# Kernel optimization log

Hardware: AMD Instinct MI355X
Metric: run time of the kernel (lower is better)

## Reference

```python
import jax, jax.numpy as jnp
import numpy as np

# architecture (from init_kwargs): layer_widths = [1024, 512, 512, 512]
D0, D1, D2, D3 = 1024, 512, 512, 512
D = D1 + D2 + D3  # flat DEQ state dim = 1536
M_AA = 5          # anderson history size
LAM = 1e-4        # tikhonov reg in least-squares
THRES = 50        # hard-coded in DeepDEQAutoencoder.forward
BETA = 1.0


def enc(z, Y, W1, W2, W3):
    """Encoder f(z, Y): z_l_new = relu(W_l @ z_{l-1}), z_0 = Y. z is [B, D]."""
    z1 = z[:, :D1]
    z2 = z[:, D1:D1 + D2]
    n1 = jax.nn.relu(Y @ W1.T)   # [B, D1]
    n2 = jax.nn.relu(z1 @ W2.T)  # [B, D2]
    n3 = jax.nn.relu(z2 @ W3.T)  # [B, D3]
    return jnp.concatenate([n1, n2, n3], axis=1)


def anderson(f, x0, m=M_AA, lam=LAM, threshold=THRES, beta=BETA):
    """Standard DEQ Anderson acceleration, fixed `threshold` iterations."""
    B, d = x0.shape
    X = jnp.zeros((B, m, d), x0.dtype)
    F = jnp.zeros((B, m, d), x0.dtype)
    f0 = f(x0)
    X = X.at[:, 0].set(x0)
    F = F.at[:, 0].set(f0)
    X = X.at[:, 1].set(f0)
    F = F.at[:, 1].set(f(f0))
    for k in range(2, threshold):
        n = min(k, m)
        G = F[:, :n] - X[:, :n]                                  # [B, n, d]
        H = jnp.einsum('bnd,bmd->bnm', G, G) + lam * jnp.eye(n, dtype=x0.dtype)
        # bordered system: [[0, 1^T], [1, H]] alpha_full = e_0
        top = jnp.concatenate([jnp.zeros((B, 1, 1), x0.dtype),
                               jnp.ones((B, 1, n), x0.dtype)], axis=2)
        bot = jnp.concatenate([jnp.ones((B, n, 1), x0.dtype), H], axis=2)
        Hf = jnp.concatenate([top, bot], axis=1)                 # [B, n+1, n+1]
        yv = jnp.zeros((B, n + 1, 1), x0.dtype).at[:, 0, 0].set(1.0)
        alpha = jnp.linalg.solve(Hf, yv)[:, 1:, 0]               # [B, n]
        xk = beta * jnp.einsum('bn,bnd->bd', alpha, F[:, :n]) \
             + (1.0 - beta) * jnp.einsum('bn,bnd->bd', alpha, X[:, :n])
        X = X.at[:, k % m].set(xk)
        F = F.at[:, k % m].set(f(xk))
    return F[:, (threshold - 1) % m]


def setup_inputs() -> dict:
    key = jax.random.key(0)
    ks = jax.random.split(key, 7)
    # weight scale 0.03 keeps the relu network contractive so the fixed point is stable
    return {
        'Y':  jax.random.normal(ks[0], (4096, D0), jnp.float32),
        'W1': jax.random.normal(ks[1], (D1, D0), jnp.float32) * 0.03,
        'W2': jax.random.normal(ks[2], (D2, D1), jnp.float32) * 0.03,
        'W3': jax.random.normal(ks[3], (D3, D2), jnp.float32) * 0.03,
        'b1': jax.random.normal(ks[4], (D0,), jnp.float32) * 0.01,
        'b2': jax.random.normal(ks[5], (D1,), jnp.float32) * 0.01,
        'b3': jax.random.normal(ks[6], (D2,), jnp.float32) * 0.01,
    }


def reference(Y, W1, W2, W3, b1, b2, b3):
    B = Y.shape[0]
    z0 = jnp.zeros((B, D), Y.dtype)
    z_star = anderson(lambda z: enc(z, Y, W1, W2, W3), z0)
    # eval mode: new_f_star = f_star; return calc_all_etas(f_star)
    z1 = z_star[:, :D1]
    z2 = z_star[:, D1:D1 + D2]
    z3 = z_star[:, D1 + D2:]
    eta1 = z1 @ W1 + b1  # linear(z_l, M_l.weight.T, biases[l]) == z_l @ W_l + b_l
    eta2 = z2 @ W2 + b2
    eta3 = z3 @ W3 + b3
    # (etas, zs) packed into one array along features: [B, 1024+512+512 + 1536]
    return jnp.concatenate([eta1, eta2, eta3, z1, z2, z3], axis=1)
```

## Files before the change

### kernel.cpp

```cpp
#include <hip/hip_runtime.h>
#include <hip/hip_bf16.h>
#include <cstdint>

#define OUT_LD 3584

typedef __bf16 bf16x8 __attribute__((ext_vector_type(8)));
typedef float  f32x4  __attribute__((ext_vector_type(4)));

__device__ __forceinline__ short f2bf(float v) {
  __hip_bfloat16 h = __float2bfloat16(v);
  return *reinterpret_cast<short*>(&h);
}

__device__ __forceinline__ void async16(const short* g, short* l) {
  __builtin_amdgcn_global_load_lds(
      (const __attribute__((address_space(1))) unsigned int*)g,
      (__attribute__((address_space(3))) unsigned int*)l, 16, 0, 0);
}

template<int BM, int WAVES_M, int WAVES_N, bool RELU>
__device__ __forceinline__ void gemm_body(
    const short* __restrict__ A, const short* __restrict__ B, int K,
    int bm, int bn, const float* __restrict__ bias,
    float* __restrict__ fout, short* __restrict__ cbf, int cld)
{
  constexpr int WM = BM / WAVES_M;
  constexpr int WN = 128 / WAVES_N;
  constexpr int MR = WM / 16;
  constexpr int NR = WN / 16;
  constexpr int PA = BM / 32;

  __shared__ __align__(16) short sA[2][BM * 64];
  __shared__ __align__(16) short sB[2][128 * 64];

  const int tid  = threadIdx.x;
  const int lane = tid & 63;
  const int wid  = tid >> 6;
  const int wr = (wid / WAVES_N) * WM;
  const int wc = (wid % WAVES_N) * WN;
  const int fr = lane & 15;
  const int fk = (lane >> 4) * 8;

  const int sr = tid >> 3;
  const int sc = (tid & 7) * 8;
  const short* ga0 = A + (size_t)(bm + sr) * K + sc;
  const short* gb0 = B + (size_t)(bn + sr) * K + sc;

  f32x4 acc[MR][NR] = {};
  const int nk = K >> 6;

  auto stage = [&](int buf, int kt) {
    const int koff = kt * 64;
    #pragma unroll
    for (int p = 0; p < PA; ++p)
      async16(ga0 + (size_t)(p * 32) * K + koff, &sA[buf][tid * 8 + p * 2048]);
    #pragma unroll
    for (int p = 0; p < 4; ++p)
      async16(gb0 + (size_t)(p * 32) * K + koff, &sB[buf][tid * 8 + p * 2048]);
  };

  stage(0, 0);
  __syncthreads();
  int cur = 0;
  for (int kt = 0; kt < nk; ++kt) {
    if (kt + 1 < nk) stage(cur ^ 1, kt + 1);
    #pragma unroll
    for (int kk = 0; kk < 2; ++kk) {
      bf16x8 a[MR], b[NR];
      #pragma unroll
      for (int i = 0; i < MR; ++i)
        a[i] = *(const bf16x8*)&sA[cur][(wr + i * 16 + fr) * 64 + kk * 32 + fk];
      #pragma unroll
      for (int j = 0; j < NR; ++j)
        b[j] = *(const bf16x8*)&sB[cur][(wc + j * 16 + fr) * 64 + kk * 32 + fk];
      #pragma unroll
      for (int i = 0; i < MR; ++i)
        #pragma unroll
        for (int j = 0; j < NR; ++j)
          acc[i][j] = __builtin_amdgcn_mfma_f32_16x16x32_bf16(a[i], b[j], acc[i][j], 0, 0, 0);
    }
    __syncthreads();
    cur ^= 1;
  }

  const int r0 = (lane >> 4) * 4;
  #pragma unroll
  for (int i = 0; i < MR; ++i) {
    #pragma unroll
    for (int j = 0; j < NR; ++j) {
      const int col = bn + wc + j * 16 + fr;
      #pragma unroll
      for (int r = 0; r < 4; ++r) {
        const int row = bm + wr + i * 16 + r0 + r;
        float v = acc[i][j][r];
        if (RELU) {
          float rv = v > 0.f ? v : 0.f;
          cbf[(size_t)row * cld + col] = f2bf(rv);
          fout[(size_t)row * OUT_LD + col] = rv;
        } else {
          fout[(size_t)row * OUT_LD + col] = v + bias[col];
        }
      }
    }
  }
}

template<int BM, int WAVES_M, int WAVES_N>
__global__ __launch_bounds__(256)
void gemm_relu(const short* __restrict__ A, const short* __restrict__ B, int K,
               float* __restrict__ zout, short* __restrict__ cbf) {
  gemm_body<BM, WAVES_M, WAVES_N, true>(A, B, K, blockIdx.x * BM, blockIdx.y * 128,
                                        nullptr, zout, cbf, 512);
}

__global__ __launch_bounds__(256)
void gemm_eta(const short* __restrict__ c1, const short* __restrict__ c2,
              const short* __restrict__ c3, const short* __restrict__ W1T,
              const short* __restrict__ W2T, const short* __restrict__ W3T,
              const float* __restrict__ b1, const float* __restrict__ b2,
              const float* __restrict__ b3, float* __restrict__ out) {
  const int b = blockIdx.x;
  const short *A, *B; const float* bias; float* eo; int l;
  if (b < 256)      { l = b;       A = c1; B = W1T; bias = b1; eo = out; }
  else if (b < 384) { l = b - 256; A = c2; B = W2T; bias = b2; eo = out + 1024; }
  else              { l = b - 384; A = c3; B = W3T; bias = b3; eo = out + 1536; }
  const int bm = (l & 31) * 128;
  const int bn = (l >> 5) * 128;
  gemm_body<128, 2, 2, false>(A, B, 512, bm, bn, bias, eo, nullptr, 0);
}

__global__ void prep_cvt(const float* __restrict__ Y, const float* __restrict__ W1,
                         const float* __restrict__ W2, const float* __restrict__ W3,
                         short* __restrict__ Ybf, short* __restrict__ W1b,
                         short* __restrict__ W2b, short* __restrict__ W3b) {
  const int i = blockIdx.x * 256 + threadIdx.x;
  const float* src; short* dst; int off;
  if (i < 1048576)      { src = Y;  dst = Ybf; off = i; }
  else if (i < 1179648) { src = W1; dst = W1b; off = i - 1048576; }
  else if (i < 1245184) { src = W2; dst = W2b; off = i - 1179648; }
  else                  { src = W3; dst = W3b; off = i - 1245184; }
  const float4 v = reinterpret_cast<const float4*>(src)[off];
  short4 o;
  o.x = f2bf(v.x); o.y = f2bf(v.y); o.z = f2bf(v.z); o.w = f2bf(v.w);
  reinterpret_cast<short4*>(dst)[off] = o;
}

__global__ void prep_tr(const float* __restrict__ W1, const float* __restrict__ W2,
                        const float* __restrict__ W3, short* __restrict__ W1T,
                        short* __restrict__ W2T, short* __restrict__ W3T) {
  __shared__ short s[32][33];
  const int b = blockIdx.x;
  const float* in; short* out; int R, C, ti, tj;
  if (b < 512)      { in = W1; out = W1T; R = 512; C = 1024; ti = b >> 5; tj = b & 31; }
  else if (b < 768) { int l = b - 512; in = W2; out = W2T; R = 512; C = 512; ti = l >> 4; tj = l & 15; }
  else              { int l = b - 768; in = W3; out = W3T; R = 512; C = 512; ti = l >> 4; tj = l & 15; }
  const int r0 = ti * 32, c0 = tj * 32;
  const int tx = threadIdx.x & 31, ty = threadIdx.x >> 5;
  #pragma unroll
  for (int q = 0; q < 4; ++q)
    s[ty + q * 8][tx] = f2bf(in[(size_t)(r0 + ty + q * 8) * C + c0 + tx]);
  __syncthreads();
  #pragma unroll
  for (int q = 0; q < 4; ++q)
    out[(size_t)(c0 + ty + q * 8) * R + r0 + tx] = s[tx][ty + q * 8];
}

extern "C" void kernel_launch(void* const* d_in, const int* in_sizes, int n_in,
                              void* d_out, int out_size, void* d_ws, size_t ws_size,
                              hipStream_t stream) {
  const float* Y  = (const float*)d_in[0];
  const float* W1 = (const float*)d_in[1];
  const float* W2 = (const float*)d_in[2];
  const float* W3 = (const float*)d_in[3];
  const float* b1 = (const float*)d_in[4];
  const float* b2 = (const float*)d_in[5];
  const float* b3 = (const float*)d_in[6];
  float* out = (float*)d_out;

  if (ws_size < 25165824) return;

  char* ws = (char*)d_ws;
  short* Ybf  = (short*)(ws);
  short* c1bf = (short*)(ws + 8388608);
  short* c2bf = (short*)(ws + 12582912);
  short* c3bf = (short*)(ws + 16777216);
  short* W1b  = (short*)(ws + 20971520);
  short* W2b  = (short*)(ws + 22020096);
  short* W3b  = (short*)(ws + 22544384);
  short* W1T  = (short*)(ws + 23068672);
  short* W2T  = (short*)(ws + 24117248);
  short* W3T  = (short*)(ws + 24641536);

  prep_cvt<<<5120, 256, 0, stream>>>(Y, W1, W2, W3, Ybf, W1b, W2b, W3b);
  prep_tr<<<1024, 256, 0, stream>>>(W1, W2, W3, W1T, W2T, W3T);

  gemm_relu<64, 1, 4><<<dim3(64, 4), 256, 0, stream>>>(Ybf, W1b, 1024, out + 2048, c1bf);
  gemm_relu<64, 1, 4><<<dim3(64, 4), 256, 0, stream>>>(c1bf, W2b, 512, out + 2560, c2bf);
  gemm_relu<64, 1, 4><<<dim3(64, 4), 256, 0, stream>>>(c2bf, W3b, 512, out + 3072, c3bf);
  gemm_eta<<<512, 256, 0, stream>>>(c1bf, c2bf, c3bf, W1T, W2T, W3T, b1, b2, b3, out);
}
```

Measured before the change: 138.8 us.

## Fuse three relu layers into one LDS-resident chain kernel and merge prep kernels

Replaces the three per-layer relu GEMM launches with a single kernel in which each 32-row block computes layer 1 from Y, keeps the bf16 activation in swizzled shared memory, and feeds it into layers 2 and 3. The two preprocessing kernels are merged into one launch, and the eta GEMM is rewritten to read operands directly from global memory instead of staging them through LDS. This aims to cut launch overhead and global round-trips of intermediate activations. The cost is lower parallelism (128 blocks) and weight reads without LDS reuse.

```diff
diff --git a/kernel.cpp b/kernel.cpp
--- a/kernel.cpp
+++ b/kernel.cpp
@@ -12,157 +12,227 @@
   return *reinterpret_cast<short*>(&h);
 }
 
-__device__ __forceinline__ void async16(const short* g, short* l) {
-  __builtin_amdgcn_global_load_lds(
-      (const __attribute__((address_space(1))) unsigned int*)g,
-      (__attribute__((address_space(3))) unsigned int*)l, 16, 0, 0);
-}
-
-template<int BM, int WAVES_M, int WAVES_N, bool RELU>
-__device__ __forceinline__ void gemm_body(
-    const short* __restrict__ A, const short* __restrict__ B, int K,
-    int bm, int bn, const float* __restrict__ bias,
-    float* __restrict__ fout, short* __restrict__ cbf, int cld)
-{
-  constexpr int WM = BM / WAVES_M;
-  constexpr int WN = 128 / WAVES_N;
-  constexpr int MR = WM / 16;
-  constexpr int NR = WN / 16;
-  constexpr int PA = BM / 32;
-
-  __shared__ __align__(16) short sA[2][BM * 64];
-  __shared__ __align__(16) short sB[2][128 * 64];
+__device__ __forceinline__ f32x4 mfma16(bf16x8 a, bf16x8 b, f32x4 c) {
+  return __builtin_amdgcn_mfma_f32_16x16x32_bf16(a, b, c, 0, 0, 0);
+}
+
+__device__ __forceinline__ void chain_epi(
+    f32x4 acc[2][4], int bm, int wc, int lane,
+    float* __restrict__ zout, short* __restrict__ cbf, char* act)
+{
+  const int fr = lane & 15;
+  const int q0 = (lane >> 4) * 4;
+  #pragma unroll
+  for (int i = 0; i < 2; ++i) {
+    #pragma unroll
+    for (int j = 0; j < 4; ++j) {
+      const int col = wc + j * 16 + fr;
+      #pragma unroll
+      for (int q = 0; q < 4; ++q) {
+        const int row = i * 16 + q0 + q;
+        float rv = acc[i][j][q];
+        rv = rv > 0.f ? rv : 0.f;
+        zout[(size_t)(bm + row) * OUT_LD + col] = rv;
+        const short bv = f2bf(rv);
+        cbf[(size_t)(bm + row) * 512 + col] = bv;
+        if (act) {
+          const int byte = ((row * 512 + col) * 2) ^ ((row & 7) << 4);
+          *(short*)(act + byte) = bv;
+        }
+      }
+    }
+  }
+}
+
+__global__ __launch_bounds__(512)
+void chain_kernel(const short* __restrict__ Ybf,
+                  const short* __restrict__ W1b, const short* __restrict__ W2b,
+                  const short* __restrict__ W3b,
+                  short* __restrict__ c1bf, short* __restrict__ c2bf,
+                  short* __restrict__ c3bf, float* __restrict__ out)
+{
+  __shared__ __align__(16) char act[32 * 512 * 2];
 
   const int tid  = threadIdx.x;
   const int lane = tid & 63;
   const int wid  = tid >> 6;
-  const int wr = (wid / WAVES_N) * WM;
-  const int wc = (wid % WAVES_N) * WN;
-  const int fr = lane & 15;
-  const int fk = (lane >> 4) * 8;
-
-  const int sr = tid >> 3;
-  const int sc = (tid & 7) * 8;
-  const short* ga0 = A + (size_t)(bm + sr) * K + sc;
-  const short* gb0 = B + (size_t)(bn + sr) * K + sc;
-
-  f32x4 acc[MR][NR] = {};
-  const int nk = K >> 6;
-
-  auto stage = [&](int buf, int kt) {
-    const int koff = kt * 64;
-    #pragma unroll
-    for (int p = 0; p < PA; ++p)
-      async16(ga0 + (size_t)(p * 32) * K + koff, &sA[buf][tid * 8 + p * 2048]);
-    #pragma unroll
-    for (int p = 0; p < 4; ++p)
-      async16(gb0 + (size_t)(p * 32) * K + koff, &sB[buf][tid * 8 + p * 2048]);
-  };
-
-  stage(0, 0);
+  const int bm   = blockIdx.x * 32;
+  const int wc   = wid * 64;
+  const int fr   = lane & 15;
+  const int fkg  = lane >> 4;
+  const int fk   = fkg * 8;
+
+  f32x4 acc[2][4];
+
+  {
+    #pragma unroll
+    for (int i = 0; i < 2; ++i)
+      #pragma unroll
+      for (int j = 0; j < 4; ++j) acc[i][j] = (f32x4){0.f, 0.f, 0.f, 0.f};
+    const short* A0 = Ybf + (size_t)(bm + fr) * 1024 + fk;
+    const short* B0 = W1b + (size_t)(wc + fr) * 1024 + fk;
+    #pragma unroll 4
+    for (int kt = 0; kt < 32; ++kt) {
+      bf16x8 a0 = *(const bf16x8*)(A0 + kt * 32);
+      bf16x8 a1 = *(const bf16x8*)(A0 + 16 * 1024 + kt * 32);
+      bf16x8 b[4];
+      #pragma unroll
+      for (int j = 0; j < 4; ++j)
+        b[j] = *(const bf16x8*)(B0 + (size_t)j * 16 * 1024 + kt * 32);
+      #pragma unroll
+      for (int j = 0; j < 4; ++j) {
+        acc[0][j] = mfma16(a0, b[j], acc[0][j]);
+        acc[1][j] = mfma16(a1, b[j], acc[1][j]);
+      }
+    }
+    chain_epi(acc, bm, wc, lane, out + 2048, c1bf, act);
+  }
   __syncthreads();
-  int cur = 0;
-  for (int kt = 0; kt < nk; ++kt) {
-    if (kt + 1 < nk) stage(cur ^ 1, kt + 1);
-    #pragma unroll
-    for (int kk = 0; kk < 2; ++kk) {
-      bf16x8 a[MR], b[NR];
-      #pragma unroll
-      for (int i = 0; i < MR; ++i)
-        a[i] = *(const bf16x8*)&sA[cur][(wr + i * 16 + fr) * 64 + kk * 32 + fk];
-      #pragma unroll
-      for (int j = 0; j < NR; ++j)
-        b[j] = *(const bf16x8*)&sB[cur][(wc + j * 16 + fr) * 64 + kk * 32 + fk];
-      #pragma unroll
-      for (int i = 0; i < MR; ++i)
-        #pragma unroll
-        for (int j = 0; j < NR; ++j)
-          acc[i][j] = __builtin_amdgcn_mfma_f32_16x16x32_bf16(a[i], b[j], acc[i][j], 0, 0, 0);
+
+  {
+    #pragma unroll
+    for (int i = 0; i < 2; ++i)
+      #pragma unroll
+      for (int j = 0; j < 4; ++j) acc[i][j] = (f32x4){0.f, 0.f, 0.f, 0.f};
+    const short* B0 = W2b + (size_t)(wc + fr) * 512 + fk;
+    #pragma unroll 4
+    for (int kt = 0; kt < 16; ++kt) {
+      const int r0 = fr, r1 = 16 + fr;
+      bf16x8 a0 = *(const bf16x8*)(act + ((r0 * 1024 + kt * 64 + fkg * 16) ^ ((r0 & 7) << 4)));
+      bf16x8 a1 = *(const bf16x8*)(act + ((r1 * 1024 + kt * 64 + fkg * 16) ^ ((r1 & 7) << 4)));
+      bf16x8 b[4];
+      #pragma unroll
+      for (int j = 0; j < 4; ++j)
+        b[j] = *(const bf16x8*)(B0 + (size_t)j * 16 * 512 + kt * 32);
+      #pragma unroll
+      for (int j = 0; j < 4; ++j) {
+        acc[0][j] = mfma16(a0, b[j], acc[0][j]);
+        acc[1][j] = mfma16(a1, b[j], acc[1][j]);
+      }
     }
     __syncthreads();
-    cur ^= 1;
-  }
-
-  const int r0 = (lane >> 4) * 4;
+    chain_epi(acc, bm, wc, lane, out + 2560, c2bf, act);
+  }
+  __syncthreads();
+
+  {
+    #pragma unroll
+    for (int i = 0; i < 2; ++i)
+      #pragma unroll
+      for (int j = 0; j < 4; ++j) acc[i][j] = (f32x4){0.f, 0.f, 0.f, 0.f};
+    const short* B0 = W3b + (size_t)(wc + fr) * 512 + fk;
+    #pragma unroll 4
+    for (int kt = 0; kt < 16; ++kt) {
+      const int r0 = fr, r1 = 16 + fr;
+      bf16x8 a0 = *(const bf16x8*)(act + ((r0 * 1024 + kt * 64 + fkg * 16) ^ ((r0 & 7) << 4)));
+      bf16x8 a1 = *(const bf16x8*)(act + ((r1 * 1024 + kt * 64 + fkg * 16) ^ ((r1 & 7) << 4)));
+      bf16x8 b[4];
+      #pragma unroll
+      for (int j = 0; j < 4; ++j)
+        b[j] = *(const bf16x8*)(B0 + (size_t)j * 16 * 512 + kt * 32);
+      #pragma unroll
+      for (int j = 0; j < 4; ++j) {
+        acc[0][j] = mfma16(a0, b[j], acc[0][j]);
+        acc[1][j] = mfma16(a1, b[j], acc[1][j]);
+      }
+    }
+    chain_epi(acc, bm, wc, lane, out + 3072, c3bf, nullptr);
+  }
+}
+
+__global__ __launch_bounds__(256)
+void eta_kernel(const short* __restrict__ c1bf, const short* __restrict__ c2bf,
+                const short* __restrict__ c3bf,
+                const short* __restrict__ W1T, const short* __restrict__ W2T,
+                const short* __restrict__ W3T,
+                const float* __restrict__ b1, const float* __restrict__ b2,
+                const float* __restrict__ b3, float* __restrict__ out)
+{
+  const int blk  = blockIdx.x;
+  const int brow = blk & 63;
+  const int bcol = blk >> 6;
+  const short* A; const short* Bw; const float* bias; int outoff, bn;
+  if (bcol < 8)       { A = c1bf; Bw = W1T; bias = b1; outoff = 0;    bn = bcol * 128; }
+  else if (bcol < 12) { A = c2bf; Bw = W2T; bias = b2; outoff = 1024; bn = (bcol - 8) * 128; }
+  else                { A = c3bf; Bw = W3T; bias = b3; outoff = 1536; bn = (bcol - 12) * 128; }
+  const int bm   = brow * 64;
+  const int tid  = threadIdx.x;
+  const int lane = tid & 63;
+  const int wid  = tid >> 6;
+  const int wr   = (wid >> 1) * 32;
+  const int wc   = (wid & 1) * 64;
+  const int fr   = lane & 15;
+  const int fk   = (lane >> 4) * 8;
+
+  f32x4 acc[2][4] = {};
+  const short* A0 = A  + (size_t)(bm + wr + fr) * 512 + fk;
+  const short* B0 = Bw + (size_t)(bn + wc + fr) * 512 + fk;
+  #pragma unroll 4
+  for (int kt = 0; kt < 16; ++kt) {
+    bf16x8 a0 = *(const bf16x8*)(A0 + kt * 32);
+    bf16x8 a1 = *(const bf16x8*)(A0 + 16 * 512 + kt * 32);
+    bf16x8 b[4];
+    #pragma unroll
+    for (int j = 0; j < 4; ++j)
+      b[j] = *(const bf16x8*)(B0 + (size_t)j * 16 * 512 + kt * 32);
+    #pragma unroll
+    for (int j = 0; j < 4; ++j) {
+      acc[0][j] = mfma16(a0, b[j], acc[0][j]);
+      acc[1][j] = mfma16(a1, b[j], acc[1][j]);
+    }
+  }
+  const int q0 = (lane >> 4) * 4;
   #pragma unroll
-  for (int i = 0; i < MR; ++i) {
-    #pragma unroll
-    for (int j = 0; j < NR; ++j) {
+  for (int i = 0; i < 2; ++i) {
+    #pragma unroll
+    for (int j = 0; j < 4; ++j) {
       const int col = bn + wc + j * 16 + fr;
-      #pragma unroll
-      for (int r = 0; r < 4; ++r) {
-        const int row = bm + wr + i * 16 + r0 + r;
-        float v = acc[i][j][r];
-        if (RELU) {
-          float rv = v > 0.f ? v : 0.f;
-          cbf[(size_t)row * cld + col] = f2bf(rv);
-          fout[(size_t)row * OUT_LD + col] = rv;
-        } else {
-          fout[(size_t)row * OUT_LD + col] = v + bias[col];
-        }
-      }
-    }
-  }
-}
-
-template<int BM, int WAVES_M, int WAVES_N>
-__global__ __launch_bounds__(256)
-void gemm_relu(const short* __restrict__ A, const short* __restrict__ B, int K,
-               float* __restrict__ zout, short* __restrict__ cbf) {
-  gemm_body<BM, WAVES_M, WAVES_N, true>(A, B, K, blockIdx.x * BM, blockIdx.y * 128,
-                                        nullptr, zout, cbf, 512);
-}
-
-__global__ __launch_bounds__(256)
-void gemm_eta(const short* __restrict__ c1, const short* __restrict__ c2,
-              const short* __restrict__ c3, const short* __restrict__ W1T,
-              const short* __restrict__ W2T, const short* __restrict__ W3T,
-              const float* __restrict__ b1, const float* __restrict__ b2,
-              const float* __restrict__ b3, float* __restrict__ out) {
-  const int b = blockIdx.x;
-  const short *A, *B; const float* bias; float* eo; int l;
-  if (b < 256)      { l = b;       A = c1; B = W1T; bias = b1; eo = out; }
-  else if (b < 384) { l = b - 256; A = c2; B = W2T; bias = b2; eo = out + 1024; }
-  else              { l = b - 384; A = c3; B = W3T; bias = b3; eo = out + 1536; }
-  const int bm = (l & 31) * 128;
-  const int bn = (l >> 5) * 128;
-  gemm_body<128, 2, 2, false>(A, B, 512, bm, bn, bias, eo, nullptr, 0);
-}
-
-__global__ void prep_cvt(const float* __restrict__ Y, const float* __restrict__ W1,
-                         const float* __restrict__ W2, const float* __restrict__ W3,
-                         short* __restrict__ Ybf, short* __restrict__ W1b,
-                         short* __restrict__ W2b, short* __restrict__ W3b) {
-  const int i = blockIdx.x * 256 + threadIdx.x;
-  const float* src; short* dst; int off;
-  if (i < 1048576)      { src = Y;  dst = Ybf; off = i; }
-  else if (i < 1179648) { src = W1; dst = W1b; off = i - 1048576; }
-  else if (i < 1245184) { src = W2; dst = W2b; off = i - 1179648; }
-  else                  { src = W3; dst = W3b; off = i - 1245184; }
-  const float4 v = reinterpret_cast<const float4*>(src)[off];
-  short4 o;
-  o.x = f2bf(v.x); o.y = f2bf(v.y); o.z = f2bf(v.z); o.w = f2bf(v.w);
-  reinterpret_cast<short4*>(dst)[off] = o;
-}
-
-__global__ void prep_tr(const float* __restrict__ W1, const float* __restrict__ W2,
-                        const float* __restrict__ W3, short* __restrict__ W1T,
-                        short* __restrict__ W2T, short* __restrict__ W3T) {
+      const float bv = bias[col];
+      #pragma unroll
+      for (int q = 0; q < 4; ++q) {
+        const int row = bm + wr + i * 16 + q0 + q;
+        out[(size_t)row * OUT_LD + outoff + col] = acc[i][j][q] + bv;
+      }
+    }
+  }
+}
+
+__global__ void prep(const float* __restrict__ Y, const float* __restrict__ W1,
+                     const float* __restrict__ W2, const float* __restrict__ W3,
+                     short* __restrict__ Ybf, short* __restrict__ W1b,
+                     short* __restrict__ W2b, short* __restrict__ W3b,
+                     short* __restrict__ W1T, short* __restrict__ W2T,
+                     short* __restrict__ W3T)
+{
   __shared__ short s[32][33];
   const int b = blockIdx.x;
-  const float* in; short* out; int R, C, ti, tj;
-  if (b < 512)      { in = W1; out = W1T; R = 512; C = 1024; ti = b >> 5; tj = b & 31; }
-  else if (b < 768) { int l = b - 512; in = W2; out = W2T; R = 512; C = 512; ti = l >> 4; tj = l & 15; }
-  else              { int l = b - 768; in = W3; out = W3T; R = 512; C = 512; ti = l >> 4; tj = l & 15; }
-  const int r0 = ti * 32, c0 = tj * 32;
-  const int tx = threadIdx.x & 31, ty = threadIdx.x >> 5;
-  #pragma unroll
-  for (int q = 0; q < 4; ++q)
-    s[ty + q * 8][tx] = f2bf(in[(size_t)(r0 + ty + q * 8) * C + c0 + tx]);
-  __syncthreads();
-  #pragma unroll
-  for (int q = 0; q < 4; ++q)
-    out[(size_t)(c0 + ty + q * 8) * R + r0 + tx] = s[tx][ty + q * 8];
+  if (b < 5120) {
+    const int i = b * 256 + threadIdx.x;
+    const float* src; short* dst; int off;
+    if (i < 1048576)      { src = Y;  dst = Ybf; off = i; }
+    else if (i < 1179648) { src = W1; dst = W1b; off = i - 1048576; }
+    else if (i < 1245184) { src = W2; dst = W2b; off = i - 1179648; }
+    else                  { src = W3; dst = W3b; off = i - 1245184; }
+    const float4 v = reinterpret_cast<const float4*>(src)[off];
+    short4 o;
+    o.x = f2bf(v.x); o.y = f2bf(v.y); o.z = f2bf(v.z); o.w = f2bf(v.w);
+    reinterpret_cast<short4*>(dst)[off] = o;
+  } else {
+    const int t = b - 5120;
+    const float* in; short* outp; int R, C, ti, tj;
+    if (t < 512)      { in = W1; outp = W1T; R = 512; C = 1024; ti = t >> 5; tj = t & 31; }
+    else if (t < 768) { int l = t - 512; in = W2; outp = W2T; R = 512; C = 512; ti = l >> 4; tj = l & 15; }
+    else              { int l = t - 768; in = W3; outp = W3T; R = 512; C = 512; ti = l >> 4; tj = l & 15; }
+    const int r0 = ti * 32, c0 = tj * 32;
+    const int tx = threadIdx.x & 31, ty = threadIdx.x >> 5;
+    #pragma unroll
+    for (int q = 0; q < 4; ++q)
+      s[ty + q * 8][tx] = f2bf(in[(size_t)(r0 + ty + q * 8) * C + c0 + tx]);
+    __syncthreads();
+    #pragma unroll
+    for (int q = 0; q < 4; ++q)
+      outp[(size_t)(c0 + ty + q * 8) * R + r0 + tx] = s[tx][ty + q * 8];
+  }
 }
 
 extern "C" void kernel_launch(void* const* d_in, const int* in_sizes, int n_in,
@@ -191,11 +261,7 @@
   short* W2T  = (short*)(ws + 24117248);
   short* W3T  = (short*)(ws + 24641536);
 
-  prep_cvt<<<5120, 256, 0, stream>>>(Y, W1, W2, W3, Ybf, W1b, W2b, W3b);
-  prep_tr<<<1024, 256, 0, stream>>>(W1, W2, W3, W1T, W2T, W3T);
-
-  gemm_relu<64, 1, 4><<<dim3(64, 4), 256, 0, stream>>>(Ybf, W1b, 1024, out + 2048, c1bf);
-  gemm_relu<64, 1, 4><<<dim3(64, 4), 256, 0, stream>>>(c1bf, W2b, 512, out + 2560, c2bf);
-  gemm_relu<64, 1, 4><<<dim3(64, 4), 256, 0, stream>>>(c2bf, W3b, 512, out + 3072, c3bf);
-  gemm_eta<<<512, 256, 0, stream>>>(c1bf, c2bf, c3bf, W1T, W2T, W3T, b1, b2, b3, out);
-}
+  prep<<<6144, 256, 0, stream>>>(Y, W1, W2, W3, Ybf, W1b, W2b, W3b, W1T, W2T, W3T);
+  chain_kernel<<<128, 512, 0, stream>>>(Ybf, W1b, W2b, W3b, c1bf, c2bf, c3bf, out);
+  eta_kernel<<<1024, 256, 0, stream>>>(c1bf, c2bf, c3bf, W1T, W2T, W3T, b1, b2, b3, out);
+}
```

After: 214.2 us. +54.3%, slower.

## Use 64x64 tiles with XOR-swizzled LDS and merge prep kernels

Applied to the files above, without the earlier changes.

Replaces the templated GEMM body with a fixed 64x64 tile (2x2 waves of 32x32), so the relu GEMMs launch 512 blocks instead of 256 and the eta GEMM launches 2048 blocks instead of 512. Shared-memory tiles are XOR-swizzled by row to cut LDS bank conflicts on the fragment reads. The two preprocessing kernels are merged into one launch to drop one launch. Smaller tiles fill more CUs but reuse each loaded operand less and add global traffic.

```diff
diff --git a/kernel.cpp b/kernel.cpp
--- a/kernel.cpp
+++ b/kernel.cpp
@@ -18,45 +18,38 @@
       (__attribute__((address_space(3))) unsigned int*)l, 16, 0, 0);
 }
 
-template<int BM, int WAVES_M, int WAVES_N, bool RELU>
-__device__ __forceinline__ void gemm_body(
+template<bool RELU>
+__device__ __forceinline__ void gemm64(
     const short* __restrict__ A, const short* __restrict__ B, int K,
-    int bm, int bn, const float* __restrict__ bias,
-    float* __restrict__ fout, short* __restrict__ cbf, int cld)
+    int bm, int bn, const float* __restrict__ bias, int outoff,
+    float* __restrict__ fout, short* __restrict__ cbf)
 {
-  constexpr int WM = BM / WAVES_M;
-  constexpr int WN = 128 / WAVES_N;
-  constexpr int MR = WM / 16;
-  constexpr int NR = WN / 16;
-  constexpr int PA = BM / 32;
-
-  __shared__ __align__(16) short sA[2][BM * 64];
-  __shared__ __align__(16) short sB[2][128 * 64];
+  __shared__ __align__(16) short sA[2][64 * 64];
+  __shared__ __align__(16) short sB[2][64 * 64];
 
   const int tid  = threadIdx.x;
   const int lane = tid & 63;
   const int wid  = tid >> 6;
-  const int wr = (wid / WAVES_N) * WM;
-  const int wc = (wid % WAVES_N) * WN;
-  const int fr = lane & 15;
-  const int fk = (lane >> 4) * 8;
+  const int wr   = (wid >> 1) * 32;
+  const int wc   = (wid & 1) * 32;
+  const int fr   = lane & 15;
+  const int fkg  = lane >> 4;
 
-  const int sr = tid >> 3;
-  const int sc = (tid & 7) * 8;
-  const short* ga0 = A + (size_t)(bm + sr) * K + sc;
-  const short* gb0 = B + (size_t)(bn + sr) * K + sc;
+  const int srow = tid >> 3;
+  const int sg   = (tid & 7) ^ (srow & 7);
+  const short* ga0 = A + (size_t)(bm + srow) * K + sg * 8;
+  const short* gb0 = B + (size_t)(bn + srow) * K + sg * 8;
 
-  f32x4 acc[MR][NR] = {};
+  f32x4 acc[2][2] = {};
   const int nk = K >> 6;
 
   auto stage = [&](int buf, int kt) {
     const int koff = kt * 64;
     #pragma unroll
-    for (int p = 0; p < PA; ++p)
-      async16(ga0 + (size_t)(p * 32) * K + koff, &sA[buf][tid * 8 + p * 2048]);
-    #pragma unroll
-    for (int p = 0; p < 4; ++p)
-      async16(gb0 + (size_t)(p * 32) * K + koff, &sB[buf][tid * 8 + p * 2048]);
+    for (int p = 0; p < 2; ++p) {
+      async16(ga0 + (size_t)(p * 32) * K + koff, &sA[buf][p * 2048 + tid * 8]);
+      async16(gb0 + (size_t)(p * 32) * K + koff, &sB[buf][p * 2048 + tid * 8]);
+    }
   };
 
   stage(0, 0);
@@ -66,51 +59,55 @@
     if (kt + 1 < nk) stage(cur ^ 1, kt + 1);
     #pragma unroll
     for (int kk = 0; kk < 2; ++kk) {
-      bf16x8 a[MR], b[NR];
+      bf16x8 a[2], b[2];
       #pragma unroll
-      for (int i = 0; i < MR; ++i)
-        a[i] = *(const bf16x8*)&sA[cur][(wr + i * 16 + fr) * 64 + kk * 32 + fk];
+      for (int i = 0; i < 2; ++i) {
+        const int row = wr + i * 16 + fr;
+        a[i] = *(const bf16x8*)((const char*)&sA[cur][0] +
+                 row * 128 + (((kk * 4 + fkg) ^ (row & 7)) * 16));
+      }
       #pragma unroll
-      for (int j = 0; j < NR; ++j)
-        b[j] = *(const bf16x8*)&sB[cur][(wc + j * 16 + fr) * 64 + kk * 32 + fk];
+      for (int j = 0; j < 2; ++j) {
+        const int row = wc + j * 16 + fr;
+        b[j] = *(const bf16x8*)((const char*)&sB[cur][0] +
+                 row * 128 + (((kk * 4 + fkg) ^ (row & 7)) * 16));
+      }
       #pragma unroll
-      for (int i = 0; i < MR; ++i)
+      for (int i = 0; i < 2; ++i)
         #pragma unroll
-        for (int j = 0; j < NR; ++j)
+        for (int j = 0; j < 2; ++j)
           acc[i][j] = __builtin_amdgcn_mfma_f32_16x16x32_bf16(a[i], b[j], acc[i][j], 0, 0, 0);
     }
     __syncthreads();
     cur ^= 1;
   }
 
-  const int r0 = (lane >> 4) * 4;
+  const int q0 = (lane >> 4) * 4;
   #pragma unroll
-  for (int i = 0; i < MR; ++i) {
+  for (int i = 0; i < 2; ++i) {
     #pragma unroll
-    for (int j = 0; j < NR; ++j) {
+    for (int j = 0; j < 2; ++j) {
       const int col = bn + wc + j * 16 + fr;
       #pragma unroll
-      for (int r = 0; r < 4; ++r) {
-        const int row = bm + wr + i * 16 + r0 + r;
-        float v = acc[i][j][r];
+      for (int q = 0; q < 4; ++q) {
+        const int row = bm + wr + i * 16 + q0 + q;
+        float v = acc[i][j][q];
         if (RELU) {
           float rv = v > 0.f ? v : 0.f;
-          cbf[(size_t)row * cld + col] = f2bf(rv);
           fout[(size_t)row * OUT_LD + col] = rv;
+          cbf[(size_t)row * 512 + col] = f2bf(rv);
         } else {
-          fout[(size_t)row * OUT_LD + col] = v + bias[col];
+          fout[(size_t)row * OUT_LD + outoff + col] = v + bias[col];
         }
       }
     }
   }
 }
 
-template<int BM, int WAVES_M, int WAVES_N>
 __global__ __launch_bounds__(256)
 void gemm_relu(const short* __restrict__ A, const short* __restrict__ B, int K,
                float* __restrict__ zout, short* __restrict__ cbf) {
-  gemm_body<BM, WAVES_M, WAVES_N, true>(A, B, K, blockIdx.x * BM, blockIdx.y * 128,
-                                        nullptr, zout, cbf, 512);
+  gemm64<true>(A, B, K, blockIdx.x * 64, blockIdx.y * 64, nullptr, 0, zout, cbf);
 }
 
 __global__ __launch_bounds__(256)
@@ -119,50 +116,50 @@
               const short* __restrict__ W2T, const short* __restrict__ W3T,
               const float* __restrict__ b1, const float* __restrict__ b2,
               const float* __restrict__ b3, float* __restrict__ out) {
-  const int b = blockIdx.x;
-  const short *A, *B; const float* bias; float* eo; int l;
-  if (b < 256)      { l = b;       A = c1; B = W1T; bias = b1; eo = out; }
-  else if (b < 384) { l = b - 256; A = c2; B = W2T; bias = b2; eo = out + 1024; }
-  else              { l = b - 384; A = c3; B = W3T; bias = b3; eo = out + 1536; }
-  const int bm = (l & 31) * 128;
-  const int bn = (l >> 5) * 128;
-  gemm_body<128, 2, 2, false>(A, B, 512, bm, bn, bias, eo, nullptr, 0);
+  const int y = blockIdx.y;
+  const short* A; const short* Bw; const float* bias; int outoff, bn;
+  if (y < 16)      { A = c1; Bw = W1T; bias = b1; outoff = 0;    bn = y * 64; }
+  else if (y < 24) { A = c2; Bw = W2T; bias = b2; outoff = 1024; bn = (y - 16) * 64; }
+  else             { A = c3; Bw = W3T; bias = b3; outoff = 1536; bn = (y - 24) * 64; }
+  gemm64<false>(A, Bw, 512, blockIdx.x * 64, bn, bias, outoff, out, nullptr);
 }
 
-__global__ void prep_cvt(const float* __restrict__ Y, const float* __restrict__ W1,
-                         const float* __restrict__ W2, const float* __restrict__ W3,
-                         short* __restrict__ Ybf, short* __restrict__ W1b,
-                         short* __restrict__ W2b, short* __restrict__ W3b) {
-  const int i = blockIdx.x * 256 + threadIdx.x;
-  const float* src; short* dst; int off;
-  if (i < 1048576)      { src = Y;  dst = Ybf; off = i; }
-  else if (i < 1179648) { src = W1; dst = W1b; off = i - 1048576; }
-  else if (i < 1245184) { src = W2; dst = W2b; off = i - 1179648; }
-  else                  { src = W3; dst = W3b; off = i - 1245184; }
-  const float4 v = reinterpret_cast<const float4*>(src)[off];
-  short4 o;
-  o.x = f2bf(v.x); o.y = f2bf(v.y); o.z = f2bf(v.z); o.w = f2bf(v.w);
-  reinterpret_cast<short4*>(dst)[off] = o;
-}
-
-__global__ void prep_tr(const float* __restrict__ W1, const float* __restrict__ W2,
-                        const float* __restrict__ W3, short* __restrict__ W1T,
-                        short* __restrict__ W2T, short* __restrict__ W3T) {
+__global__ void prep(const float* __restrict__ Y, const float* __restrict__ W1,
+                     const float* __restrict__ W2, const float* __restrict__ W3,
+                     short* __restrict__ Ybf, short* __restrict__ W1b,
+                     short* __restrict__ W2b, short* __restrict__ W3b,
+                     short* __restrict__ W1T, short* __restrict__ W2T,
+                     short* __restrict__ W3T)
+{
   __shared__ short s[32][33];
   const int b = blockIdx.x;
-  const float* in; short* out; int R, C, ti, tj;
-  if (b < 512)      { in = W1; out = W1T; R = 512; C = 1024; ti = b >> 5; tj = b & 31; }
-  else if (b < 768) { int l = b - 512; in = W2; out = W2T; R = 512; C = 512; ti = l >> 4; tj = l & 15; }
-  else              { int l = b - 768; in = W3; out = W3T; R = 512; C = 512; ti = l >> 4; tj = l & 15; }
-  const int r0 = ti * 32, c0 = tj * 32;
-  const int tx = threadIdx.x & 31, ty = threadIdx.x >> 5;
-  #pragma unroll
-  for (int q = 0; q < 4; ++q)
-    s[ty + q * 8][tx] = f2bf(in[(size_t)(r0 + ty + q * 8) * C + c0 + tx]);
-  __syncthreads();
-  #pragma unroll
-  for (int q = 0; q < 4; ++q)
-    out[(size_t)(c0 + ty + q * 8) * R + r0 + tx] = s[tx][ty + q * 8];
+  if (b < 5120) {
+    const int i = b * 256 + threadIdx.x;
+    const float* src; short* dst; int off;
+    if (i < 1048576)      { src = Y;  dst = Ybf; off = i; }
+    else if (i < 1179648) { src = W1; dst = W1b; off = i - 1048576; }
+    else if (i < 1245184) { src = W2; dst = W2b; off = i - 1179648; }
+    else                  { src = W3; dst = W3b; off = i - 1245184; }
+    const float4 v = reinterpret_cast<const float4*>(src)[off];
+    short4 o;
+    o.x = f2bf(v.x); o.y = f2bf(v.y); o.z = f2bf(v.z); o.w = f2bf(v.w);
+    reinterpret_cast<short4*>(dst)[off] = o;
+  } else {
+    const int t = b - 5120;
+    const float* in; short* outp; int R, C, ti, tj;
+    if (t < 512)      { in = W1; outp = W1T; R = 512; C = 1024; ti = t >> 5; tj = t & 31; }
+    else if (t < 768) { int l = t - 512; in = W2; outp = W2T; R = 512; C = 512; ti = l >> 4; tj = l & 15; }
+    else              { int l = t - 768; in = W3; outp = W3T; R = 512; C = 512; ti = l >> 4; tj = l & 15; }
+    const int r0 = ti * 32, c0 = tj * 32;
+    const int tx = threadIdx.x & 31, ty = threadIdx.x >> 5;
+    #pragma unroll
+    for (int q = 0; q < 4; ++q)
+      s[ty + q * 8][tx] = f2bf(in[(size_t)(r0 + ty + q * 8) * C + c0 + tx]);
+    __syncthreads();
+    #pragma unroll
+    for (int q = 0; q < 4; ++q)
+      outp[(size_t)(c0 + ty + q * 8) * R + r0 + tx] = s[tx][ty + q * 8];
+  }
 }
 
 extern "C" void kernel_launch(void* const* d_in, const int* in_sizes, int n_in,
@@ -191,11 +188,10 @@
   short* W2T  = (short*)(ws + 24117248);
   short* W3T  = (short*)(ws + 24641536);
 
-  prep_cvt<<<5120, 256, 0, stream>>>(Y, W1, W2, W3, Ybf, W1b, W2b, W3b);
-  prep_tr<<<1024, 256, 0, stream>>>(W1, W2, W3, W1T, W2T, W3T);
+  prep<<<6144, 256, 0, stream>>>(Y, W1, W2, W3, Ybf, W1b, W2b, W3b, W1T, W2T, W3T);
 
-  gemm_relu<64, 1, 4><<<dim3(64, 4), 256, 0, stream>>>(Ybf, W1b, 1024, out + 2048, c1bf);
-  gemm_relu<64, 1, 4><<<dim3(64, 4), 256, 0, stream>>>(c1bf, W2b, 512, out + 2560, c2bf);
-  gemm_relu<64, 1, 4><<<dim3(64, 4), 256, 0, stream>>>(c2bf, W3b, 512, out + 3072, c3bf);
-  gemm_eta<<<512, 256, 0, stream>>>(c1bf, c2bf, c3bf, W1T, W2T, W3T, b1, b2, b3, out);
+  gemm_relu<<<dim3(64, 8), 256, 0, stream>>>(Ybf, W1b, 1024, out + 2048, c1bf);
+  gemm_relu<<<dim3(64, 8), 256, 0, stream>>>(c1bf, W2b, 512, out + 2560, c2bf);
+  gemm_relu<<<dim3(64, 8), 256, 0, stream>>>(c2bf, W3b, 512, out + 3072, c3bf);
+  gemm_eta<<<dim3(64, 32), 256, 0, stream>>>(c1bf, c2bf, c3bf, W1T, W2T, W3T, b1, b2, b3, out);
 }
```

Result: faster. 135.9 us (-2.1%).
